# Kernel optimization log

Measured on AMD Instinct MI355X. Metric: run time of the kernel, lower is better.

Reference implementation:

```python
import jax, jax.numpy as jnp
import numpy as np

B, L, F, H = 8, 1024, 1024, 16
D = F // H  # feat_head = 64
EPS = 1e-5


def setup_inputs() -> dict:
    key = jax.random.key(0)
    ks = jax.random.split(key, 12)
    s = 1.0 / np.sqrt(F)
    inp = {
        "q": jax.random.normal(ks[0], (B, L, F), jnp.float32),
        "k": jax.random.normal(ks[1], (B, L, F), jnp.float32),
        "v": jax.random.normal(ks[2], (B, L, F), jnp.float32),
        "Wq": jax.random.uniform(ks[3], (F, F), jnp.float32, -s, s),
        "bq": jax.random.uniform(ks[4], (F,), jnp.float32, -s, s),
        "Wk": jax.random.uniform(ks[5], (F, F), jnp.float32, -s, s),
        "bk": jax.random.uniform(ks[6], (F,), jnp.float32, -s, s),
        "Wv": jax.random.uniform(ks[7], (F, F), jnp.float32, -s, s),
        "bv": jax.random.uniform(ks[8], (F,), jnp.float32, -s, s),
        "Wf": jax.random.uniform(ks[9], (F, F), jnp.float32, -s, s),
        "bf": jax.random.uniform(ks[10], (F,), jnp.float32, -s, s),
        "gamma": jnp.ones((F,), jnp.float32),
        "beta": jnp.zeros((F,), jnp.float32),
    }
    return inp


def _split_heads(x):
    # (B, L, F) -> (B*H, L, D), matching reshape->transpose(1,2)->reshape
    return x.reshape(B, L, H, D).transpose(0, 2, 1, 3).reshape(B * H, L, D)


def reference(q, k, v, Wq, bq, Wk, bk, Wv, bv, Wf, bf, gamma, beta):
    residual = q
    qh = _split_heads(q @ Wq.T + bq)
    kh = _split_heads(k @ Wk.T + bk)
    vh = _split_heads(v @ Wv.T + bv)
    # scores: (B*H, L, L)
    scores = jnp.einsum('nqd,nkd->nqk', qh, kh) / np.sqrt(D)
    raw_att = jax.nn.softmax(scores, axis=-1)
    att = jnp.einsum('nqk,nkd->nqd', raw_att, vh)  # (B*H, L, D)
    # faithful to original output recombine: reshape(H, B, L, D).permute(1,2,0,3)
    att = att.reshape(H, B, L, D).transpose(1, 2, 0, 3).reshape(B, L, F)
    att = att @ Wf.T + bf
    # dropout in eval mode = identity; activation is None
    x = att + residual
    mu = jnp.mean(x, axis=-1, keepdims=True)
    var = jnp.mean(jnp.square(x - mu), axis=-1, keepdims=True)
    out = (x - mu) * jax.lax.rsqrt(var + EPS) * gamma + beta
    return out, raw_att
```

## Files before the change

### kernel.cpp

```cpp
#include <hip/hip_runtime.h>

#define BB 8
#define LL 1024
#define FF 1024
#define HH 16
#define DD 64
#define NBH 128

typedef __attribute__((ext_vector_type(8))) short bf16x8;
typedef __attribute__((ext_vector_type(4))) float f32x4;

#define GLD_LDS16(g, l)                                                        \
  __builtin_amdgcn_global_load_lds(                                            \
      (const __attribute__((address_space(1))) unsigned int*)(g),              \
      (__attribute__((address_space(3))) unsigned int*)(l), 16, 0, 0)

__device__ __forceinline__ unsigned short f2bf(float f) {
  unsigned int u = __float_as_uint(f);
  unsigned int r = u + 0x7fffu + ((u >> 16) & 1u);
  return (unsigned short)(r >> 16);
}
__device__ __forceinline__ float bf2f(unsigned short s) {
  return __uint_as_float(((unsigned int)s) << 16);
}

__global__ __launch_bounds__(256) void cvt_all(
    const float* __restrict__ q, const float* __restrict__ k,
    const float* __restrict__ v, const float* __restrict__ w0,
    const float* __restrict__ w1, const float* __restrict__ w2,
    const float* __restrict__ w3, short* __restrict__ dst) {
  const int NA = (BB * LL * FF) / 4;
  const int NW = (FF * FF) / 4;
  int i = blockIdx.x * 256 + threadIdx.x;
  const float* src;
  int off;
  if (i < 3 * NA) {
    int z = i >> 21;
    src = (z == 0) ? q : (z == 1) ? k : v;
    off = i - z * NA;
  } else {
    int j = i - 3 * NA;
    int z = j >> 18;
    src = (z == 0) ? w0 : (z == 1) ? w1 : (z == 2) ? w2 : w3;
    off = j - z * NW;
  }
  f32x4 val = __builtin_nontemporal_load((const f32x4*)src + off);
  short4 o;
  o.x = (short)f2bf(val[0]); o.y = (short)f2bf(val[1]);
  o.z = (short)f2bf(val[2]); o.w = (short)f2bf(val[3]);
  ((short4*)dst)[i] = o;
}

__global__ __launch_bounds__(256) void proj_qkv(
    const short* __restrict__ Aall, const short* __restrict__ Wall,
    const float* __restrict__ bq, const float* __restrict__ bk,
    const float* __restrict__ bv, short* __restrict__ Dall) {
  const int o = blockIdx.x + (blockIdx.y << 6) + (blockIdx.z << 9);
  const int n = ((o & 7) * 192) + (o >> 3);
  const int z = n >> 9;
  const int r = n & 511;
  const int by = r & 7, bx = r >> 3;

  const short* A  = Aall + (size_t)z * (BB * LL * FF);
  const short* Bt = Wall + (size_t)z * (FF * FF);
  const float* bias = (z == 0) ? bq : (z == 1) ? bk : bv;
  short* dst = Dall + (size_t)z * ((size_t)NBH * LL * DD);
  const float scale = (z == 0) ? 0.125f * 1.44269504088896f : 1.0f;

  __shared__ __attribute__((aligned(16))) short LB[128 * 136];
  short* As = LB;
  short* Bs = LB + 128 * 64;

  const int tid = threadIdx.x;
  const int lane = tid & 63, w = tid >> 6;
  const int wr = w >> 1, wc = w & 1;
  const int row16 = lane & 15, kg = lane >> 4;
  const int m0 = bx * 128, n0 = by * 128;

  const f32x4 z4 = {0.f, 0.f, 0.f, 0.f};
  f32x4 acc[4][4];
  for (int i = 0; i < 4; ++i)
    for (int j = 0; j < 4; ++j) acc[i][j] = z4;

  for (int k0 = 0; k0 < FF; k0 += 64) {
#pragma unroll
    for (int rr = 0; rr < 4; ++rr) {
      int e8 = tid + rr * 256;
      int row = e8 >> 3, cs = ((e8 & 7) ^ (row & 7)) * 8;
      GLD_LDS16(A + (size_t)(m0 + row) * FF + k0 + cs, As + e8 * 8);
      GLD_LDS16(Bt + (size_t)(n0 + row) * FF + k0 + cs, Bs + e8 * 8);
    }
    __syncthreads();
#pragma unroll
    for (int kk2 = 0; kk2 < 2; ++kk2) {
      bf16x8 af[4], bfr[4];
#pragma unroll
      for (int i = 0; i < 4; ++i) {
        int ra = wr * 64 + i * 16 + row16;
        int rb = wc * 64 + i * 16 + row16;
        af[i]  = *(const bf16x8*)(As + ra * 64 + ((((kk2 << 2) | kg) ^ (ra & 7)) << 3));
        bfr[i] = *(const bf16x8*)(Bs + rb * 64 + ((((kk2 << 2) | kg) ^ (rb & 7)) << 3));
      }
#pragma unroll
      for (int i = 0; i < 4; ++i)
#pragma unroll
        for (int j = 0; j < 4; ++j)
          acc[i][j] = __builtin_amdgcn_mfma_f32_16x16x32_bf16(af[i], bfr[j], acc[i][j], 0, 0, 0);
    }
    __syncthreads();
  }

  const int z2 = (z == 2);
#pragma unroll
  for (int i = 0; i < 4; ++i) {
#pragma unroll
    for (int j = 0; j < 4; ++j) {
      int nl = wc * 64 + j * 16 + row16;
      float bn = bias[n0 + nl];
#pragma unroll
      for (int rr = 0; rr < 4; ++rr) {
        int ml = wr * 64 + i * 16 + kg * 4 + rr;
        float val = (acc[i][j][rr] + bn) * scale;
        int rrow = z2 ? nl : ml, ccol = z2 ? ml : nl;
        LB[rrow * 136 + ccol] = (short)f2bf(val);
      }
    }
  }
  __syncthreads();
  const int b = m0 >> 10;
  const int lbase = m0 & 1023;
#pragma unroll
  for (int rr = 0; rr < 8; ++rr) {
    int e = tid + rr * 256;
    int row = e >> 4, c8 = e & 15;
    uint4 val = *(const uint4*)(LB + row * 136 + c8 * 8);
    if (!z2) {
      int l = lbase + row;
      int h = (n0 + c8 * 8) >> 6, d = (c8 & 7) * 8;
      *(uint4*)(dst + (((size_t)(b * HH + h)) * LL + l) * DD + d) = val;
    } else {
      int h = (n0 + row) >> 6, d = (n0 + row) & 63;
      int l = lbase + c8 * 8;
      *(uint4*)(dst + (((size_t)(b * HH + h)) * DD + d) * LL + l) = val;
    }
  }
}

__global__ __launch_bounds__(256) void attn_kernel(
    const short* __restrict__ Qh, const short* __restrict__ Kh,
    const short* __restrict__ Vt, float* __restrict__ Patt,
    short* __restrict__ attb) {
  const int o = blockIdx.x + (blockIdx.y << 4);
  const int n = ((o & 7) << 8) + (o >> 3);
  const int bh = n >> 4;
  const int q0 = (n & 15) * 64;
  const int tid = threadIdx.x;
  const int lane = tid & 63, w = tid >> 6;
  const int row16 = lane & 15, kg = lane >> 4;

  __shared__ __attribute__((aligned(16))) short Qs[64 * 64];
  __shared__ __attribute__((aligned(16))) short Ks[2][64 * 64];
  __shared__ __attribute__((aligned(16))) short Vts[2][64 * 64];
  __shared__ __attribute__((aligned(16))) short PsT[4][16 * 64];

  auto kbuf3 = [&](int i) -> short* {
    return (i == 2) ? &Vts[0][0] : &Ks[i][0];
  };

#define STAGE_K(tt, dstp)                                                      \
  {                                                                            \
    int e8a = tid, rowa = e8a >> 3, c8a = (e8a & 7) ^ (rowa & 7);              \
    GLD_LDS16(Kh + ((size_t)bh * LL + (tt) * 64 + rowa) * DD + c8a * 8,        \
              (dstp) + e8a * 8);                                               \
    int e8b = tid + 256, rowb = e8b >> 3, c8b = (e8b & 7) ^ (rowb & 7);        \
    GLD_LDS16(Kh + ((size_t)bh * LL + (tt) * 64 + rowb) * DD + c8b * 8,        \
              (dstp) + e8b * 8);                                               \
  }
#define STAGE_V(tt, dstp)                                                      \
  {                                                                            \
    int e8a = tid, rowa = e8a >> 3, c8a = (e8a & 7) ^ (rowa & 7);              \
    GLD_LDS16(Vt + ((size_t)bh * DD + rowa) * LL + (tt) * 64 + c8a * 8,        \
              (dstp) + e8a * 8);                                               \
    int e8b = tid + 256, rowb = e8b >> 3, c8b = (e8b & 7) ^ (rowb & 7);        \
    GLD_LDS16(Vt + ((size_t)bh * DD + rowb) * LL + (tt) * 64 + c8b * 8,        \
              (dstp) + e8b * 8);                                               \
  }

  {
    int e8a = tid, rowa = e8a >> 3, c8a = (e8a & 7) ^ (rowa & 7);
    GLD_LDS16(Qh + ((size_t)bh * LL + q0 + rowa) * DD + c8a * 8, Qs + e8a * 8);
    int e8b = tid + 256, rowb = e8b >> 3, c8b = (e8b & 7) ^ (rowb & 7);
    GLD_LDS16(Qh + ((size_t)bh * LL + q0 + rowb) * DD + c8b * 8, Qs + e8b * 8);
  }
  STAGE_K(0, kbuf3(0));
  STAGE_K(1, kbuf3(1));
  asm volatile("s_waitcnt vmcnt(2)" ::: "memory");
  __builtin_amdgcn_s_barrier();

  const int qrow = w * 16 + row16;
  bf16x8 aq0 = *(const bf16x8*)(Qs + qrow * 64 + ((kg ^ (qrow & 7)) << 3));
  bf16x8 aq1 = *(const bf16x8*)(Qs + qrow * 64 + (((kg + 4) ^ (qrow & 7)) << 3));

  const f32x4 z4 = {0.f, 0.f, 0.f, 0.f};
  float lsum = 0.f;

  for (int t = 0; t < 16; ++t) {
    const short* kb = kbuf3(t % 3);
    if (t < 14) {
      short* kd = kbuf3((t + 2) % 3);
      STAGE_K(t + 2, kd);
    }
    f32x4 s[4] = {z4, z4, z4, z4};
    __builtin_amdgcn_s_setprio(1);
#pragma unroll
    for (int tt = 0; tt < 4; ++tt) {
      int krow = tt * 16 + row16;
      bf16x8 b0 = *(const bf16x8*)(kb + krow * 64 + ((kg ^ (krow & 7)) << 3));
      bf16x8 b1 = *(const bf16x8*)(kb + krow * 64 + (((kg + 4) ^ (krow & 7)) << 3));
      s[tt] = __builtin_amdgcn_mfma_f32_16x16x32_bf16(b0, aq0, s[tt], 0, 0, 0);
      s[tt] = __builtin_amdgcn_mfma_f32_16x16x32_bf16(b1, aq1, s[tt], 0, 0, 0);
    }
    __builtin_amdgcn_s_setprio(0);
#pragma unroll
    for (int tt = 0; tt < 4; ++tt)
#pragma unroll
      for (int rr = 0; rr < 4; ++rr) lsum += exp2f(s[tt][rr]);
    if (t < 14) {
      asm volatile("s_waitcnt vmcnt(2)" ::: "memory");
    } else {
      asm volatile("s_waitcnt vmcnt(0)" ::: "memory");
    }
    __builtin_amdgcn_s_barrier();
  }
  lsum += __shfl_xor(lsum, 16);
  lsum += __shfl_xor(lsum, 32);
  const float lc = __log2f(lsum);

  f32x4 oT[4] = {z4, z4, z4, z4};

  STAGE_K(0, &Ks[0][0]);
  STAGE_V(0, &Vts[0][0]);
  asm volatile("s_waitcnt vmcnt(0)" ::: "memory");
  __builtin_amdgcn_s_barrier();
  for (int t = 0; t < 16; ++t) {
    const int cur = t & 1;
    if (t < 15) {
      STAGE_K(t + 1, &Ks[cur ^ 1][0]);
      STAGE_V(t + 1, &Vts[cur ^ 1][0]);
    }
    f32x4 s[4] = {z4, z4, z4, z4};
    __builtin_amdgcn_s_setprio(1);
#pragma unroll
    for (int tt = 0; tt < 4; ++tt) {
      int krow = tt * 16 + row16;
      bf16x8 b0 = *(const bf16x8*)(&Ks[cur][krow * 64 + ((kg ^ (krow & 7)) << 3)]);
      bf16x8 b1 = *(const bf16x8*)(&Ks[cur][krow * 64 + (((kg + 4) ^ (krow & 7)) << 3)]);
      s[tt] = __builtin_amdgcn_mfma_f32_16x16x32_bf16(b0, aq0, s[tt], 0, 0, 0);
      s[tt] = __builtin_amdgcn_mfma_f32_16x16x32_bf16(b1, aq1, s[tt], 0, 0, 0);
    }
    __builtin_amdgcn_s_setprio(0);
    const int qq = q0 + w * 16 + row16;
    const int k0 = t * 64;
#pragma unroll
    for (int tt = 0; tt < 4; ++tt) {
      f32x4 pv;
#pragma unroll
      for (int rr = 0; rr < 4; ++rr) pv[rr] = exp2f(s[tt][rr] - lc);
      __builtin_nontemporal_store(
          pv, (f32x4*)(Patt + ((size_t)bh * LL + qq) * LL + k0 + tt * 16 + kg * 4));
      short4 ps;
      ps.x = (short)f2bf(pv[0]); ps.y = (short)f2bf(pv[1]);
      ps.z = (short)f2bf(pv[2]); ps.w = (short)f2bf(pv[3]);
      int c = ((tt * 2 + (kg >> 1)) ^ (row16 & 7));
      *(short4*)(&PsT[w][row16 * 64 + c * 8 + (kg & 1) * 4]) = ps;
    }
    bf16x8 pb0 = *(const bf16x8*)(&PsT[w][row16 * 64 + ((kg ^ (row16 & 7)) << 3)]);
    bf16x8 pb1 = *(const bf16x8*)(&PsT[w][row16 * 64 + (((4 + kg) ^ (row16 & 7)) << 3)]);
    __builtin_amdgcn_s_setprio(1);
#pragma unroll
    for (int td = 0; td < 4; ++td) {
      int trow = td * 16 + row16;
      bf16x8 v0 = *(const bf16x8*)(&Vts[cur][trow * 64 + ((kg ^ (trow & 7)) << 3)]);
      bf16x8 v1 = *(const bf16x8*)(&Vts[cur][trow * 64 + (((kg + 4) ^ (trow & 7)) << 3)]);
      oT[td] = __builtin_amdgcn_mfma_f32_16x16x32_bf16(v0, pb0, oT[td], 0, 0, 0);
      oT[td] = __builtin_amdgcn_mfma_f32_16x16x32_bf16(v1, pb1, oT[td], 0, 0, 0);
    }
    __builtin_amdgcn_s_setprio(0);
    if (t < 15) {
      asm volatile("s_waitcnt vmcnt(4)" ::: "memory");
      __builtin_amdgcn_s_barrier();
    }
  }

  const int iblk = bh >> 3;
  const int jb = bh & 7;
  const int qq = q0 + w * 16 + row16;
#pragma unroll
  for (int td = 0; td < 4; ++td) {
    short4 ov;
    ov.x = (short)f2bf(oT[td][0]); ov.y = (short)f2bf(oT[td][1]);
    ov.z = (short)f2bf(oT[td][2]); ov.w = (short)f2bf(oT[td][3]);
    *(short4*)(attb + ((size_t)jb * LL + qq) * FF + iblk * 64 + td * 16 + kg * 4) = ov;
  }
#undef STAGE_K
#undef STAGE_V
}

__global__ __launch_bounds__(256) void proj_out(
    const short* __restrict__ A, const short* __restrict__ Bt,
    const float* __restrict__ bias, const short* __restrict__ resid,
    short* __restrict__ xb) {
  const int o = blockIdx.x + (blockIdx.y << 6);
  const int n = ((o & 7) << 6) + (o >> 3);
  const int by = n & 7, bx = n >> 3;

  __shared__ __attribute__((aligned(16))) short As[128 * 64];
  __shared__ __attribute__((aligned(16))) short Bs[128 * 64];

  const int tid = threadIdx.x;
  const int lane = tid & 63, w = tid >> 6;
  const int wr = w >> 1, wc = w & 1;
  const int row16 = lane & 15, kg = lane >> 4;
  const int m0 = bx * 128, n0 = by * 128;

  const f32x4 z4 = {0.f, 0.f, 0.f, 0.f};
  f32x4 acc[4][4];
  for (int i = 0; i < 4; ++i)
    for (int j = 0; j < 4; ++j) acc[i][j] = z4;

  for (int k0 = 0; k0 < FF; k0 += 64) {
#pragma unroll
    for (int rr = 0; rr < 4; ++rr) {
      int e8 = tid + rr * 256;
      int row = e8 >> 3, cs = ((e8 & 7) ^ (row & 7)) * 8;
      GLD_LDS16(A + (size_t)(m0 + row) * FF + k0 + cs, As + e8 * 8);
      GLD_LDS16(Bt + (size_t)(n0 + row) * FF + k0 + cs, Bs + e8 * 8);
    }
    __syncthreads();
#pragma unroll
    for (int kk2 = 0; kk2 < 2; ++kk2) {
      bf16x8 af[4], bfr[4];
#pragma unroll
      for (int i = 0; i < 4; ++i) {
        int ra = wr * 64 + i * 16 + row16;
        int rb = wc * 64 + i * 16 + row16;
        af[i]  = *(const bf16x8*)(As + ra * 64 + ((((kk2 << 2) | kg) ^ (ra & 7)) << 3));
        bfr[i] = *(const bf16x8*)(Bs + rb * 64 + ((((kk2 << 2) | kg) ^ (rb & 7)) << 3));
      }
#pragma unroll
      for (int i = 0; i < 4; ++i)
#pragma unroll
        for (int j = 0; j < 4; ++j)
          acc[i][j] = __builtin_amdgcn_mfma_f32_16x16x32_bf16(af[i], bfr[j], acc[i][j], 0, 0, 0);
    }
    __syncthreads();
  }

#pragma unroll
  for (int i = 0; i < 4; ++i) {
#pragma unroll
    for (int j = 0; j < 4; ++j) {
      int ncol = n0 + wc * 64 + j * 16 + row16;
      float bn = bias[ncol];
#pragma unroll
      for (int rr = 0; rr < 4; ++rr) {
        int m = m0 + wr * 64 + i * 16 + kg * 4 + rr;
        float val = acc[i][j][rr] + bn + bf2f((unsigned short)resid[(size_t)m * FF + ncol]);
        xb[(size_t)m * FF + ncol] = (short)f2bf(val);
      }
    }
  }
}

__global__ __launch_bounds__(256) void ln_kernel(const short* __restrict__ xb,
                                                 const float* __restrict__ gamma,
                                                 const float* __restrict__ beta,
                                                 float* __restrict__ out) {
  const int row = blockIdx.x;
  const int tid = threadIdx.x;
  const short4 v4 = *(const short4*)(xb + (size_t)row * FF + tid * 4);
  float vx = bf2f((unsigned short)v4.x), vy = bf2f((unsigned short)v4.y);
  float vz = bf2f((unsigned short)v4.z), vw = bf2f((unsigned short)v4.w);
  float s = vx + vy + vz + vw;
  float s2 = vx * vx + vy * vy + vz * vz + vw * vw;
#pragma unroll
  for (int o = 1; o < 64; o <<= 1) {
    s += __shfl_xor(s, o);
    s2 += __shfl_xor(s2, o);
  }
  __shared__ float ss[4], ss2[4];
  int w = tid >> 6, lane = tid & 63;
  if (lane == 0) { ss[w] = s; ss2[w] = s2; }
  __syncthreads();
  s = ss[0] + ss[1] + ss[2] + ss[3];
  s2 = ss2[0] + ss2[1] + ss2[2] + ss2[3];
  float mu = s * (1.0f / 1024.0f);
  float var = s2 * (1.0f / 1024.0f) - mu * mu;
  float rs = rsqrtf(var + 1e-5f);
  float4 g = *(const float4*)(gamma + tid * 4);
  float4 be = *(const float4*)(beta + tid * 4);
  f32x4 o;
  o[0] = (vx - mu) * rs * g.x + be.x;
  o[1] = (vy - mu) * rs * g.y + be.y;
  o[2] = (vz - mu) * rs * g.z + be.z;
  o[3] = (vw - mu) * rs * g.w + be.w;
  __builtin_nontemporal_store(o, (f32x4*)(out + (size_t)row * FF + tid * 4));
}

extern "C" void kernel_launch(void* const* d_in, const int* in_sizes, int n_in,
                              void* d_out, int out_size, void* d_ws, size_t ws_size,
                              hipStream_t stream) {
  const float* q  = (const float*)d_in[0];
  const float* k  = (const float*)d_in[1];
  const float* v  = (const float*)d_in[2];
  const float* Wq = (const float*)d_in[3];
  const float* bq = (const float*)d_in[4];
  const float* Wk = (const float*)d_in[5];
  const float* bk = (const float*)d_in[6];
  const float* Wv = (const float*)d_in[7];
  const float* bv = (const float*)d_in[8];
  const float* Wf = (const float*)d_in[9];
  const float* bf = (const float*)d_in[10];
  const float* gamma = (const float*)d_in[11];
  const float* beta  = (const float*)d_in[12];

  float* out = (float*)d_out;
  float* Patt = out + (size_t)BB * LL * FF;

  char* ws = (char*)d_ws;
  const size_t MB = (size_t)1 << 20;
  short* qb = (short*)(ws + 0 * MB);
  short* Wb = (short*)(ws + 48 * MB);
  short* Qh = (short*)(ws + 56 * MB);
  short* Kh = (short*)(ws + 72 * MB);
  short* Vt = (short*)(ws + 88 * MB);
  short* attb = (short*)(ws + 32 * MB);
  short* xb = (short*)(ws + 16 * MB);

  cvt_all<<<28672, 256, 0, stream>>>(q, k, v, Wq, Wk, Wv, Wf, qb);

  proj_qkv<<<dim3(64, 8, 3), 256, 0, stream>>>(qb, Wb, bq, bk, bv, Qh);
  attn_kernel<<<dim3(16, 128), 256, 0, stream>>>(Qh, Kh, Vt, Patt, attb);
  proj_out<<<dim3(64, 8), 256, 0, stream>>>(attb, Wb + 3 * (size_t)FF * FF, bf, qb, xb);
  ln_kernel<<<8192, 256, 0, stream>>>(xb, gamma, beta, out);
}
```

Baseline: 290.1 us.

## Load K/V operands directly from global memory instead of staging through LDS

The attention kernel stops staging Q, K and V tiles into shared memory with async global-to-LDS loads, multi-buffering and barriers. Each wave now reads its MFMA operands straight from global memory and relies on the caches, with loops unrolled by two. This removes barrier synchronisation and LDS traffic and frees LDS, which may raise occupancy. In exchange every wave issues its own redundant global loads of the shared K/V tiles, and there is no explicit prefetch to hide that latency.

```diff
diff --git a/kernel.cpp b/kernel.cpp
--- a/kernel.cpp
+++ b/kernel.cpp
@@ -158,65 +158,28 @@
   const int lane = tid & 63, w = tid >> 6;
   const int row16 = lane & 15, kg = lane >> 4;
 
-  __shared__ __attribute__((aligned(16))) short Qs[64 * 64];
-  __shared__ __attribute__((aligned(16))) short Ks[2][64 * 64];
-  __shared__ __attribute__((aligned(16))) short Vts[2][64 * 64];
   __shared__ __attribute__((aligned(16))) short PsT[4][16 * 64];
 
-  auto kbuf3 = [&](int i) -> short* {
-    return (i == 2) ? &Vts[0][0] : &Ks[i][0];
-  };
-
-#define STAGE_K(tt, dstp)                                                      \
-  {                                                                            \
-    int e8a = tid, rowa = e8a >> 3, c8a = (e8a & 7) ^ (rowa & 7);              \
-    GLD_LDS16(Kh + ((size_t)bh * LL + (tt) * 64 + rowa) * DD + c8a * 8,        \
-              (dstp) + e8a * 8);                                               \
-    int e8b = tid + 256, rowb = e8b >> 3, c8b = (e8b & 7) ^ (rowb & 7);        \
-    GLD_LDS16(Kh + ((size_t)bh * LL + (tt) * 64 + rowb) * DD + c8b * 8,        \
-              (dstp) + e8b * 8);                                               \
-  }
-#define STAGE_V(tt, dstp)                                                      \
-  {                                                                            \
-    int e8a = tid, rowa = e8a >> 3, c8a = (e8a & 7) ^ (rowa & 7);              \
-    GLD_LDS16(Vt + ((size_t)bh * DD + rowa) * LL + (tt) * 64 + c8a * 8,        \
-              (dstp) + e8a * 8);                                               \
-    int e8b = tid + 256, rowb = e8b >> 3, c8b = (e8b & 7) ^ (rowb & 7);        \
-    GLD_LDS16(Vt + ((size_t)bh * DD + rowb) * LL + (tt) * 64 + c8b * 8,        \
-              (dstp) + e8b * 8);                                               \
-  }
-
-  {
-    int e8a = tid, rowa = e8a >> 3, c8a = (e8a & 7) ^ (rowa & 7);
-    GLD_LDS16(Qh + ((size_t)bh * LL + q0 + rowa) * DD + c8a * 8, Qs + e8a * 8);
-    int e8b = tid + 256, rowb = e8b >> 3, c8b = (e8b & 7) ^ (rowb & 7);
-    GLD_LDS16(Qh + ((size_t)bh * LL + q0 + rowb) * DD + c8b * 8, Qs + e8b * 8);
-  }
-  STAGE_K(0, kbuf3(0));
-  STAGE_K(1, kbuf3(1));
-  asm volatile("s_waitcnt vmcnt(2)" ::: "memory");
-  __builtin_amdgcn_s_barrier();
-
   const int qrow = w * 16 + row16;
-  bf16x8 aq0 = *(const bf16x8*)(Qs + qrow * 64 + ((kg ^ (qrow & 7)) << 3));
-  bf16x8 aq1 = *(const bf16x8*)(Qs + qrow * 64 + (((kg + 4) ^ (qrow & 7)) << 3));
+  const short* qp = Qh + ((size_t)bh * LL + q0 + qrow) * DD;
+  bf16x8 aq0 = *(const bf16x8*)(qp + kg * 8);
+  bf16x8 aq1 = *(const bf16x8*)(qp + 32 + kg * 8);
+
+  const short* Kb = Kh + (size_t)bh * LL * DD;
+  const short* Vb = Vt + (size_t)bh * DD * LL;
 
   const f32x4 z4 = {0.f, 0.f, 0.f, 0.f};
   float lsum = 0.f;
 
+#pragma unroll 2
   for (int t = 0; t < 16; ++t) {
-    const short* kb = kbuf3(t % 3);
-    if (t < 14) {
-      short* kd = kbuf3((t + 2) % 3);
-      STAGE_K(t + 2, kd);
-    }
     f32x4 s[4] = {z4, z4, z4, z4};
     __builtin_amdgcn_s_setprio(1);
 #pragma unroll
     for (int tt = 0; tt < 4; ++tt) {
-      int krow = tt * 16 + row16;
-      bf16x8 b0 = *(const bf16x8*)(kb + krow * 64 + ((kg ^ (krow & 7)) << 3));
-      bf16x8 b1 = *(const bf16x8*)(kb + krow * 64 + (((kg + 4) ^ (krow & 7)) << 3));
+      const short* kp = Kb + (size_t)(t * 64 + tt * 16 + row16) * DD;
+      bf16x8 b0 = *(const bf16x8*)(kp + kg * 8);
+      bf16x8 b1 = *(const bf16x8*)(kp + 32 + kg * 8);
       s[tt] = __builtin_amdgcn_mfma_f32_16x16x32_bf16(b0, aq0, s[tt], 0, 0, 0);
       s[tt] = __builtin_amdgcn_mfma_f32_16x16x32_bf16(b1, aq1, s[tt], 0, 0, 0);
     }
@@ -225,42 +188,28 @@
     for (int tt = 0; tt < 4; ++tt)
 #pragma unroll
       for (int rr = 0; rr < 4; ++rr) lsum += exp2f(s[tt][rr]);
-    if (t < 14) {
-      asm volatile("s_waitcnt vmcnt(2)" ::: "memory");
-    } else {
-      asm volatile("s_waitcnt vmcnt(0)" ::: "memory");
-    }
-    __builtin_amdgcn_s_barrier();
   }
   lsum += __shfl_xor(lsum, 16);
   lsum += __shfl_xor(lsum, 32);
   const float lc = __log2f(lsum);
 
   f32x4 oT[4] = {z4, z4, z4, z4};
-
-  STAGE_K(0, &Ks[0][0]);
-  STAGE_V(0, &Vts[0][0]);
-  asm volatile("s_waitcnt vmcnt(0)" ::: "memory");
-  __builtin_amdgcn_s_barrier();
+  const int qq = q0 + qrow;
+
+#pragma unroll 2
   for (int t = 0; t < 16; ++t) {
-    const int cur = t & 1;
-    if (t < 15) {
-      STAGE_K(t + 1, &Ks[cur ^ 1][0]);
-      STAGE_V(t + 1, &Vts[cur ^ 1][0]);
-    }
+    const int k0 = t * 64;
     f32x4 s[4] = {z4, z4, z4, z4};
     __builtin_amdgcn_s_setprio(1);
 #pragma unroll
     for (int tt = 0; tt < 4; ++tt) {
-      int krow = tt * 16 + row16;
-      bf16x8 b0 = *(const bf16x8*)(&Ks[cur][krow * 64 + ((kg ^ (krow & 7)) << 3)]);
-      bf16x8 b1 = *(const bf16x8*)(&Ks[cur][krow * 64 + (((kg + 4) ^ (krow & 7)) << 3)]);
+      const short* kp = Kb + (size_t)(k0 + tt * 16 + row16) * DD;
+      bf16x8 b0 = *(const bf16x8*)(kp + kg * 8);
+      bf16x8 b1 = *(const bf16x8*)(kp + 32 + kg * 8);
       s[tt] = __builtin_amdgcn_mfma_f32_16x16x32_bf16(b0, aq0, s[tt], 0, 0, 0);
       s[tt] = __builtin_amdgcn_mfma_f32_16x16x32_bf16(b1, aq1, s[tt], 0, 0, 0);
     }
     __builtin_amdgcn_s_setprio(0);
-    const int qq = q0 + w * 16 + row16;
-    const int k0 = t * 64;
 #pragma unroll
     for (int tt = 0; tt < 4; ++tt) {
       f32x4 pv;
@@ -279,22 +228,17 @@
     __builtin_amdgcn_s_setprio(1);
 #pragma unroll
     for (int td = 0; td < 4; ++td) {
-      int trow = td * 16 + row16;
-      bf16x8 v0 = *(const bf16x8*)(&Vts[cur][trow * 64 + ((kg ^ (trow & 7)) << 3)]);
-      bf16x8 v1 = *(const bf16x8*)(&Vts[cur][trow * 64 + (((kg + 4) ^ (trow & 7)) << 3)]);
+      const short* vp = Vb + (size_t)(td * 16 + row16) * LL + k0;
+      bf16x8 v0 = *(const bf16x8*)(vp + kg * 8);
+      bf16x8 v1 = *(const bf16x8*)(vp + 32 + kg * 8);
       oT[td] = __builtin_amdgcn_mfma_f32_16x16x32_bf16(v0, pb0, oT[td], 0, 0, 0);
       oT[td] = __builtin_amdgcn_mfma_f32_16x16x32_bf16(v1, pb1, oT[td], 0, 0, 0);
     }
     __builtin_amdgcn_s_setprio(0);
-    if (t < 15) {
-      asm volatile("s_waitcnt vmcnt(4)" ::: "memory");
-      __builtin_amdgcn_s_barrier();
-    }
   }
 
   const int iblk = bh >> 3;
   const int jb = bh & 7;
-  const int qq = q0 + w * 16 + row16;
 #pragma unroll
   for (int td = 0; td < 4; ++td) {
     short4 ov;
@@ -302,8 +246,6 @@
     ov.z = (short)f2bf(oT[td][2]); ov.w = (short)f2bf(oT[td][3]);
     *(short4*)(attb + ((size_t)jb * LL + qq) * FF + iblk * 64 + td * 16 + kg * 4) = ov;
   }
-#undef STAGE_K
-#undef STAGE_V
 }
 
 __global__ __launch_bounds__(256) void proj_out(
```

Result: slower. 486.5 us (+67.7%).
